# Kernel tuning notes

Measured on AMD Instinct MI355X. Metric: run time of the kernel, lower is better.

The kernel has to match this reference:

```python
import math
import jax, jax.numpy as jnp
import numpy as np

N, B, C, H, K = 1024, 8, 512, 8, 5  # seq len, batch, d_model, heads, near_kth
NEG = -1.0e9


def setup_inputs() -> dict:
    key = jax.random.key(0)
    ks = jax.random.split(key, 10)
    s = 0.02
    return {
        "query": jax.random.normal(ks[0], (N, B, C), jnp.float32),
        "key_t": jax.random.normal(ks[1], (N, B, C), jnp.float32),
        "value": jax.random.normal(ks[2], (N, B, C), jnp.float32),
        "src_position": jax.random.normal(ks[3], (N, B, 3), jnp.float32),
        "tgt_position": jax.random.normal(ks[4], (N, B, 3), jnp.float32),
        # nn.MultiheadAttention params (in_proj split into q/k/v, plus out_proj)
        "Wq": jax.random.normal(ks[5], (C, C), jnp.float32) * s,
        "Wk": jax.random.normal(ks[6], (C, C), jnp.float32) * s,
        "Wv": jax.random.normal(ks[7], (C, C), jnp.float32) * s,
        "bq": jnp.zeros((C,), jnp.float32),
        "bk": jnp.zeros((C,), jnp.float32),
        "bv": jnp.zeros((C,), jnp.float32),
        "Wo": jax.random.normal(ks[8], (C, C), jnp.float32) * s,
        "bo": jnp.zeros((C,), jnp.float32),
    }


def reference(query, key_t, value, src_position, tgt_position,
              Wq, Wk, Wv, bq, bk, bv, Wo, bo):
    # --- 'nearby' positional mask ---------------------------------------
    # dist[b, tgt, src] = ||src_position[src,b] - tgt_position[tgt,b]||^2
    diff = src_position[None, :, :, :] - tgt_position[:, None, :, :]  # (Nt,Ns,B,3)
    dist = jnp.sum(diff * diff, axis=-1).transpose(2, 0, 1)           # (B,Nt,Ns)
    # torch: topk(dist, k=5, dim=1, largest=False) -> 5 nearest TARGETS per source
    _, idx = jax.lax.top_k(-dist.transpose(0, 2, 1), K)               # (B,Ns,K) tgt idx
    mask = jnp.full((B, N, N), NEG, jnp.float32)
    b_i = jnp.arange(B)[:, None, None]
    s_i = jnp.arange(N)[None, :, None]
    mask = mask.at[b_i, idx, s_i].set(0.0)                            # (B,Nt,Ns)

    # --- multihead attention (eval mode, dropout=0) ----------------------
    hd = C // H
    scale = 1.0 / math.sqrt(hd)
    q = ((query @ Wq.T + bq) * scale).reshape(N, B, H, hd)
    k = (key_t @ Wk.T + bk).reshape(N, B, H, hd)
    v = (value @ Wv.T + bv).reshape(N, B, H, hd)
    scores = jnp.einsum('tbhd,sbhd->bhts', q, k) + mask[:, None]      # (B,H,Nt,Ns)
    attn = jax.nn.softmax(scores, axis=-1)
    ctx = jnp.einsum('bhts,sbhd->tbhd', attn, v).reshape(N, B, C)
    out = ctx @ Wo.T + bo                                             # (N,B,C)
    attn_avg = attn.mean(axis=1)                                      # (B,Nt,Ns)
    return out, attn_avg
```

## Files before the change

kernel.cpp:

```cpp
#include <hip/hip_runtime.h>
#include <cstdint>
#include <cstddef>

#define NSEQ 1024
#define BATCH 8
#define CMODEL 512
#define NHEAD 8
#define HDIM 64
#define CAP 64
#define FLTMAX 3.402823466e+38f

typedef short bf16x8 __attribute__((ext_vector_type(8)));
typedef float f32x4 __attribute__((ext_vector_type(4)));
typedef unsigned short ushort8v __attribute__((ext_vector_type(8)));
typedef unsigned short ushort2v __attribute__((ext_vector_type(2)));

__device__ inline unsigned short f2bf(float f) {
    unsigned int u = __builtin_bit_cast(unsigned int, f);
    u += 0x7fffu + ((u >> 16) & 1u);
    return (unsigned short)(u >> 16);
}
__device__ inline float bf2f(unsigned short u) {
    return __builtin_bit_cast(float, (unsigned int)u << 16);
}

#define GLDS16(gsrc, ldst) \
    __builtin_amdgcn_global_load_lds((const __attribute__((address_space(1))) void*)(gsrc), \
                                     (__attribute__((address_space(3))) void*)(ldst), 16, 0, 0)

__global__ __launch_bounds__(256) void convert_all(
        const float* __restrict__ a0, const float* __restrict__ a1,
        const float* __restrict__ a2,
        const float* __restrict__ w0, const float* __restrict__ w1,
        const float* __restrict__ w2, const float* __restrict__ w3,
        unsigned short* __restrict__ oa0, unsigned short* __restrict__ oa1,
        unsigned short* __restrict__ oa2,
        unsigned short* __restrict__ ow0, unsigned short* __restrict__ ow1,
        unsigned short* __restrict__ ow2, unsigned short* __restrict__ ow3,
        unsigned int* __restrict__ zp) {
    const unsigned int idx = blockIdx.x * 256 + threadIdx.x;
    if (idx >= 1703936u) { zp[idx - 1703936u] = 0u; return; }
    const float* src; unsigned short* dst; unsigned int c;
    if (idx < 1572864u) {
        const unsigned int seg = idx >> 19; c = idx & 524287u;
        src = seg == 0 ? a0 : seg == 1 ? a1 : a2;
        dst = seg == 0 ? oa0 : seg == 1 ? oa1 : oa2;
    } else {
        const unsigned int rel = idx - 1572864u, seg = rel >> 15; c = rel & 32767u;
        src = seg == 0 ? w0 : seg == 1 ? w1 : seg == 2 ? w2 : w3;
        dst = seg == 0 ? ow0 : seg == 1 ? ow1 : seg == 2 ? ow2 : ow3;
    }
    const float4 v0 = *(const float4*)(src + (size_t)c * 8);
    const float4 v1 = *(const float4*)(src + (size_t)c * 8 + 4);
    ushort8v u;
    u[0] = f2bf(v0.x); u[1] = f2bf(v0.y); u[2] = f2bf(v0.z); u[3] = f2bf(v0.w);
    u[4] = f2bf(v1.x); u[5] = f2bf(v1.y); u[6] = f2bf(v1.z); u[7] = f2bf(v1.w);
    *(ushort8v*)(dst + (size_t)c * 8) = u;
}

__global__ __launch_bounds__(256) void topk_scatter(const float* __restrict__ srcp,
                                                    const float* __restrict__ tgtp,
                                                    int* __restrict__ row_cnt,
                                                    int* __restrict__ row_list) {
    const int w = threadIdx.x >> 6, lane = threadIdx.x & 63;
    const int wg = blockIdx.x * 4 + w;
    const int s = wg & 1023, b = wg >> 10;

    const float sx = srcp[((size_t)s * BATCH + b) * 3 + 0];
    const float sy = srcp[((size_t)s * BATCH + b) * 3 + 1];
    const float sz = srcp[((size_t)s * BATCH + b) * 3 + 2];

    float dv[16];
    #pragma unroll
    for (int i = 0; i < 16; ++i) {
        const int t = i * 64 + lane;
        const float dx = tgtp[((size_t)t * BATCH + b) * 3 + 0] - sx;
        const float dy = tgtp[((size_t)t * BATCH + b) * 3 + 1] - sy;
        const float dz = tgtp[((size_t)t * BATCH + b) * 3 + 2] - sz;
        dv[i] = dx * dx + dy * dy + dz * dz;
    }

    #pragma unroll
    for (int k = 0; k < 5; ++k) {
        float bvv = FLTMAX;
        int   bii = 0x7fffffff;
        #pragma unroll
        for (int i = 0; i < 16; ++i) {
            if (dv[i] < bvv) { bvv = dv[i]; bii = i * 64 + lane; }
        }
        #pragma unroll
        for (int off = 1; off < 64; off <<= 1) {
            const float ov = __shfl_xor(bvv, off);
            const int   oi = __shfl_xor(bii, off);
            if (ov < bvv || (ov == bvv && oi < bii)) { bvv = ov; bii = oi; }
        }
        if (lane == (bii & 63)) {
            #pragma unroll
            for (int i = 0; i < 16; ++i)
                if (bii == i * 64 + lane) dv[i] = FLTMAX;
        }
        if (lane == 0) {
            const int pos = atomicAdd(&row_cnt[b * NSEQ + bii], 1);
            if (pos < CAP) row_list[((size_t)b * NSEQ + bii) * CAP + pos] = s;
        }
    }
}

template<int OMODE>
__device__ inline void gemm_body(const unsigned short* __restrict__ Abf,
                                 const unsigned short* __restrict__ Wbf,
                                 const float* __restrict__ bias,
                                 void* __restrict__ outp, float scale) {
    __shared__ __align__(16) unsigned short smem[3 * 8192];
    const int tid = threadIdx.x;
    const int l = tid & 63, w = tid >> 6;
    const int m0 = blockIdx.x * 128, n0 = blockIdx.y * 128;
    const int wr = (w >> 1) * 64, wc = (w & 1) * 64;
    const int lr = l & 15, g = l >> 4;

    f32x4 acc[4][4] = {};

    const int rowX = tid >> 2;
    const int kg0  = (tid & 3) ^ ((rowX >> 1) & 3);
    const unsigned short* aS0 = Abf + (size_t)(m0 + rowX) * CMODEL + kg0 * 8;
    const unsigned short* aS1 = aS0 + (size_t)64 * CMODEL;
    const unsigned short* bS0 = Wbf + (size_t)(n0 + rowX) * CMODEL + kg0 * 8;
    const unsigned short* bS1 = bS0 + (size_t)64 * CMODEL;
    const int wb = w * 512;

    auto STAGE = [&](int k0, int buf) {
        unsigned short* bb = smem + buf * 8192;
        GLDS16(aS0 + k0, bb + wb);
        GLDS16(aS1 + k0, bb + 2048 + wb);
        GLDS16(bS0 + k0, bb + 4096 + wb);
        GLDS16(bS1 + k0, bb + 6144 + wb);
    };
    auto COMPUTE = [&](const unsigned short* base) {
        bf16x8 af[4], bg[4];
        #pragma unroll
        for (int i = 0; i < 4; ++i) {
            const int ra = wr + i * 16 + lr;
            af[i] = *(const bf16x8*)(base + ra * 32 + ((g ^ ((ra >> 1) & 3)) << 3));
        }
        #pragma unroll
        for (int j = 0; j < 4; ++j) {
            const int rb = wc + j * 16 + lr;
            bg[j] = *(const bf16x8*)(base + 4096 + rb * 32 + ((g ^ ((rb >> 1) & 3)) << 3));
        }
        __builtin_amdgcn_s_setprio(1);
        #pragma unroll
        for (int i = 0; i < 4; ++i)
            #pragma unroll
            for (int j = 0; j < 4; ++j)
                acc[i][j] = __builtin_amdgcn_mfma_f32_16x16x32_bf16(af[i], bg[j], acc[i][j], 0, 0, 0);
        __builtin_amdgcn_s_setprio(0);
    };

    STAGE(0, 0);
    STAGE(32, 1);

    int cur = 0;
    for (int t = 0; t < 15; ++t) {
        asm volatile("s_waitcnt vmcnt(4)" ::: "memory");
        __builtin_amdgcn_s_barrier();
        if (t < 14) {
            int nb = cur + 2; if (nb >= 3) nb -= 3;
            STAGE((t + 2) * 32, nb);
        }
        COMPUTE(smem + cur * 8192);
        ++cur; if (cur == 3) cur = 0;
    }
    asm volatile("s_waitcnt vmcnt(0)" ::: "memory");
    __builtin_amdgcn_s_barrier();
    COMPUTE(smem + cur * 8192);

    #pragma unroll
    for (int i = 0; i < 4; ++i) {
        #pragma unroll
        for (int j = 0; j < 4; ++j) {
            const int col = n0 + wc + j * 16 + lr;
            const float bcol = bias[col];
            #pragma unroll
            for (int r = 0; r < 4; ++r) {
                const int row = m0 + wr + i * 16 + g * 4 + r;
                const float val = (acc[i][j][r] + bcol) * scale;
                if constexpr (OMODE == 0) {
                    const int t = row >> 3, bb = row & 7;
                    ((unsigned short*)outp)[((size_t)(bb * NSEQ + t)) * CMODEL + col] = f2bf(val);
                } else {
                    ((float*)outp)[(size_t)row * CMODEL + col] = val;
                }
            }
        }
    }
}

__global__ __launch_bounds__(256, 3) void gemm_proj(const unsigned short* __restrict__ Aq,
                                                    const unsigned short* __restrict__ Ak,
                                                    const unsigned short* __restrict__ Av,
                                                    const unsigned short* __restrict__ Wq,
                                                    const unsigned short* __restrict__ Wk,
                                                    const unsigned short* __restrict__ Wv,
                                                    const float* __restrict__ bq,
                                                    const float* __restrict__ bk,
                                                    const float* __restrict__ bv,
                                                    unsigned short* __restrict__ oq,
                                                    unsigned short* __restrict__ ok,
                                                    unsigned short* __restrict__ ov) {
    const int z = blockIdx.z;
    const unsigned short* A = z == 0 ? Aq : z == 1 ? Ak : Av;
    const unsigned short* W = z == 0 ? Wq : z == 1 ? Wk : Wv;
    const float* bi = z == 0 ? bq : z == 1 ? bk : bv;
    unsigned short* o = z == 0 ? oq : z == 1 ? ok : ov;
    const float sc = z == 0 ? 0.125f : 1.0f;
    gemm_body<0>(A, W, bi, o, sc);
}

__global__ __launch_bounds__(256, 3) void gemm_out(const unsigned short* __restrict__ Abf,
                                                   const unsigned short* __restrict__ Wbf,
                                                   const float* __restrict__ bias,
                                                   float* __restrict__ out) {
    gemm_body<1>(Abf, Wbf, bias, out, 1.0f);
}

__global__ __launch_bounds__(512) void v_mean_k(const unsigned short* __restrict__ v,
                                                float* __restrict__ vm) {
    const int b = blockIdx.x;
    const int chunk = blockIdx.y;
    const int c = threadIdx.x;
    float s = 0.f;
    const int t0 = chunk * 64;
    for (int t = 0; t < 64; ++t)
        s += bf2f(v[((size_t)b * NSEQ + t0 + t) * CMODEL + c]);
    atomicAdd(&vm[b * CMODEL + c], s * (1.f / (float)NSEQ));
}

__global__ __launch_bounds__(256) void sparse_attn(const unsigned short* __restrict__ q_ws,
                                                   const unsigned short* __restrict__ k_ws,
                                                   const unsigned short* __restrict__ v_ws,
                                                   const int* __restrict__ row_cnt,
                                                   const int* __restrict__ row_list,
                                                   const float* __restrict__ vm,
                                                   unsigned short* __restrict__ ctx,
                                                   float* __restrict__ attn_out) {
    const int t = blockIdx.x;
    const int b = blockIdx.y;
    const int tid = threadIdx.x;

    int cnt = row_cnt[b * NSEQ + t];
    if (cnt > CAP) cnt = CAP;

    float* arow = attn_out + ((size_t)b * NSEQ + t) * NSEQ;

    if (cnt == 0) {
        const float u = 1.f / (float)NSEQ;
        const float4 uv = {u, u, u, u};
        ((float4*)arow)[tid] = uv;
        for (int c = tid; c < CMODEL; c += 256)
            ctx[((size_t)t * BATCH + b) * CMODEL + c] = f2bf(vm[b * CMODEL + c]);
        return;
    }

    {
        const float4 zv = {0.f, 0.f, 0.f, 0.f};
        ((float4*)arow)[tid] = zv;
    }

    __shared__ float qs[CMODEL];
    __shared__ float esc[CAP][8];
    __shared__ float denom[8];
    __shared__ int   slist[CAP];

    if (tid < 8) denom[tid] = 0.f;
    if (tid < cnt) slist[tid] = row_list[((size_t)b * NSEQ + t) * CAP + tid];
    {
        const ushort2v qv = *(const ushort2v*)(q_ws + ((size_t)b * NSEQ + t) * CMODEL + tid * 2);
        qs[tid * 2] = bf2f(qv[0]); qs[tid * 2 + 1] = bf2f(qv[1]);
    }
    __syncthreads();

    const int wid = tid >> 6, lane = tid & 63;
    for (int i = wid; i < cnt; i += 4) {
        const int s = slist[i];
        const ushort8v kv = *(const ushort8v*)(k_ws + ((size_t)b * NSEQ + s) * CMODEL + lane * 8);
        const float* qrow = qs + lane * 8;
        float part = 0.f;
        #pragma unroll
        for (int j = 0; j < 8; ++j) part += qrow[j] * bf2f(kv[j]);
        part += __shfl_xor(part, 1);
        part += __shfl_xor(part, 2);
        part += __shfl_xor(part, 4);
        if ((lane & 7) == 0) {
            const int h = lane >> 3;
            const float e = __expf(part);
            esc[i][h] = e;
            atomicAdd(&denom[h], e);
        }
    }
    __syncthreads();

    for (int x = tid; x < cnt * 8; x += 256)
        esc[x >> 3][x & 7] /= denom[x & 7];
    __syncthreads();

    for (int i = tid; i < cnt; i += 256) {
        float pm = 0.f;
        #pragma unroll
        for (int h = 0; h < 8; ++h) pm += esc[i][h];
        arow[slist[i]] = pm * 0.125f;
    }

    const int c0 = tid * 2;
    const int h0 = c0 >> 6;
    float acc0 = 0.f, acc1 = 0.f;
    for (int i = 0; i < cnt; ++i) {
        const int s = slist[i];
        const float p = esc[i][h0];
        const ushort2v vv = *(const ushort2v*)(v_ws + ((size_t)b * NSEQ + s) * CMODEL + c0);
        acc0 += p * bf2f(vv[0]); acc1 += p * bf2f(vv[1]);
    }
    unsigned short* crow = ctx + ((size_t)t * BATCH + b) * CMODEL;
    ushort2v cv; cv[0] = f2bf(acc0); cv[1] = f2bf(acc1);
    *(ushort2v*)(crow + c0) = cv;
}

extern "C" void kernel_launch(void* const* d_in, const int* in_sizes, int n_in,
                              void* d_out, int out_size, void* d_ws, size_t ws_size,
                              hipStream_t stream) {
    (void)in_sizes; (void)n_in; (void)out_size; (void)ws_size;

    const float* query = (const float*)d_in[0];
    const float* key_t = (const float*)d_in[1];
    const float* value = (const float*)d_in[2];
    const float* srcp  = (const float*)d_in[3];
    const float* tgtp  = (const float*)d_in[4];
    const float* Wq    = (const float*)d_in[5];
    const float* Wk    = (const float*)d_in[6];
    const float* Wv    = (const float*)d_in[7];
    const float* bq    = (const float*)d_in[8];
    const float* bk    = (const float*)d_in[9];
    const float* bv    = (const float*)d_in[10];
    const float* Wo    = (const float*)d_in[11];
    const float* bo    = (const float*)d_in[12];

    float* out      = (float*)d_out;
    float* attn_out = out + (size_t)NSEQ * BATCH * CMODEL;

    const size_t NBC = (size_t)BATCH * NSEQ * CMODEL;
    const size_t WSZ = (size_t)CMODEL * CMODEL;
    unsigned short* q_ws  = (unsigned short*)d_ws;
    unsigned short* k_ws  = q_ws + NBC;
    unsigned short* v_ws  = k_ws + NBC;
    unsigned short* ctxbf = v_ws + NBC;
    unsigned short* qbf   = ctxbf + NBC;
    unsigned short* kbf   = qbf + NBC;
    unsigned short* vbf   = kbf + NBC;
    unsigned short* wqbf  = vbf + NBC;
    unsigned short* wkbf  = wqbf + WSZ;
    unsigned short* wvbf  = wkbf + WSZ;
    unsigned short* wobf  = wvbf + WSZ;
    int*   row_cnt  = (int*)(wobf + WSZ);
    float* vm       = (float*)(row_cnt + BATCH * NSEQ);
    int*   row_list = (int*)(vm + BATCH * CMODEL);

    convert_all<<<6704, 256, 0, stream>>>(query, key_t, value, Wq, Wk, Wv, Wo,
                                          qbf, kbf, vbf, wqbf, wkbf, wvbf, wobf,
                                          (unsigned int*)row_cnt);

    topk_scatter<<<2048, 256, 0, stream>>>(srcp, tgtp, row_cnt, row_list);

    gemm_proj<<<dim3(64, 4, 3), 256, 0, stream>>>(qbf, kbf, vbf,
                                                  wqbf, wkbf, wvbf,
                                                  bq, bk, bv,
                                                  q_ws, k_ws, v_ws);

    v_mean_k<<<dim3(BATCH, 16), 512, 0, stream>>>(v_ws, vm);

    sparse_attn<<<dim3(NSEQ, BATCH), 256, 0, stream>>>(q_ws, k_ws, v_ws, row_cnt,
                                                       row_list, vm, ctxbf, attn_out);

    gemm_out<<<dim3(64, 4), 256, 0, stream>>>(ctxbf, wobf, bo, out);
}
```

Before: 90.86 us.

## Fuse fp32-to-bf16 activation conversion into projection GEMM and fold V-mean

Drops the separate conversion pass over query/key/value activations. The projection GEMM now loads fp32 A tiles into registers, converts them to bf16 and writes them to LDS, while the weights are still staged through async global-to-LDS loads. The mean of V is no longer read back from the projected output. Instead the prep kernel reduces the raw fp32 value over the sequence, and an extra column of GEMM blocks multiplies that mean by Wv. This removes one full-tensor write and read plus a kernel launch, at the cost of register-path A loads, an lgkmcnt wait before every barrier, and a changed rounding of the V mean.

```diff
diff --git a/kernel.cpp b/kernel.cpp
--- a/kernel.cpp
+++ b/kernel.cpp
@@ -28,34 +28,51 @@
     __builtin_amdgcn_global_load_lds((const __attribute__((address_space(1))) void*)(gsrc), \
                                      (__attribute__((address_space(3))) void*)(ldst), 16, 0, 0)
 
-__global__ __launch_bounds__(256) void convert_all(
-        const float* __restrict__ a0, const float* __restrict__ a1,
-        const float* __restrict__ a2,
-        const float* __restrict__ w0, const float* __restrict__ w1,
-        const float* __restrict__ w2, const float* __restrict__ w3,
-        unsigned short* __restrict__ oa0, unsigned short* __restrict__ oa1,
-        unsigned short* __restrict__ oa2,
-        unsigned short* __restrict__ ow0, unsigned short* __restrict__ ow1,
-        unsigned short* __restrict__ ow2, unsigned short* __restrict__ ow3,
-        unsigned int* __restrict__ zp) {
-    const unsigned int idx = blockIdx.x * 256 + threadIdx.x;
-    if (idx >= 1703936u) { zp[idx - 1703936u] = 0u; return; }
-    const float* src; unsigned short* dst; unsigned int c;
-    if (idx < 1572864u) {
-        const unsigned int seg = idx >> 19; c = idx & 524287u;
-        src = seg == 0 ? a0 : seg == 1 ? a1 : a2;
-        dst = seg == 0 ? oa0 : seg == 1 ? oa1 : oa2;
-    } else {
-        const unsigned int rel = idx - 1572864u, seg = rel >> 15; c = rel & 32767u;
-        src = seg == 0 ? w0 : seg == 1 ? w1 : seg == 2 ? w2 : w3;
-        dst = seg == 0 ? ow0 : seg == 1 ? ow1 : seg == 2 ? ow2 : ow3;
-    }
-    const float4 v0 = *(const float4*)(src + (size_t)c * 8);
-    const float4 v1 = *(const float4*)(src + (size_t)c * 8 + 4);
-    ushort8v u;
-    u[0] = f2bf(v0.x); u[1] = f2bf(v0.y); u[2] = f2bf(v0.z); u[3] = f2bf(v0.w);
-    u[4] = f2bf(v1.x); u[5] = f2bf(v1.y); u[6] = f2bf(v1.z); u[7] = f2bf(v1.w);
-    *(ushort8v*)(dst + (size_t)c * 8) = u;
+__global__ __launch_bounds__(256) void prep(const float* __restrict__ w0,
+                                            const float* __restrict__ w1,
+                                            const float* __restrict__ w2,
+                                            const float* __restrict__ w3,
+                                            const float* __restrict__ value,
+                                            unsigned short* __restrict__ o0,
+                                            unsigned short* __restrict__ o1,
+                                            unsigned short* __restrict__ o2,
+                                            unsigned short* __restrict__ o3,
+                                            unsigned int* __restrict__ zp,
+                                            float* __restrict__ vm_raw) {
+    const int bid = blockIdx.x;
+    const int tid = threadIdx.x;
+    if (bid < 512) {
+        const int idx = bid * 256 + tid;
+        const int seg = idx >> 15;
+        const int c   = idx & 32767;
+        const float* src = seg == 0 ? w0 : seg == 1 ? w1 : seg == 2 ? w2 : w3;
+        unsigned short* dst = seg == 0 ? o0 : seg == 1 ? o1 : seg == 2 ? o2 : o3;
+        const float4 v0 = *(const float4*)(src + (size_t)c * 8);
+        const float4 v1 = *(const float4*)(src + (size_t)c * 8 + 4);
+        ushort8v u;
+        u[0] = f2bf(v0.x); u[1] = f2bf(v0.y); u[2] = f2bf(v0.z); u[3] = f2bf(v0.w);
+        u[4] = f2bf(v1.x); u[5] = f2bf(v1.y); u[6] = f2bf(v1.z); u[7] = f2bf(v1.w);
+        *(ushort8v*)(dst + (size_t)c * 8) = u;
+        return;
+    }
+    if (bid < 544) {
+        zp[(bid - 512) * 256 + tid] = 0u;
+        return;
+    }
+    const int cb = bid - 544;
+    const int b = cb >> 3, cg = cb & 7;
+    const int ts = tid >> 6, c = cg * 64 + (tid & 63);
+    float s = 0.f;
+    for (int i = 0; i < 256; ++i) {
+        const int t = ts * 256 + i;
+        s += value[((size_t)t * BATCH + b) * CMODEL + c];
+    }
+    __shared__ float sh[4][64];
+    sh[ts][tid & 63] = s;
+    __syncthreads();
+    if (ts == 0)
+        vm_raw[b * CMODEL + c] = sh[0][tid & 63] + sh[1][tid & 63] +
+                                 sh[2][tid & 63] + sh[3][tid & 63];
 }
 
 __global__ __launch_bounds__(256) void topk_scatter(const float* __restrict__ srcp,
@@ -106,11 +123,11 @@
     }
 }
 
-template<int OMODE>
-__device__ inline void gemm_body(const unsigned short* __restrict__ Abf,
-                                 const unsigned short* __restrict__ Wbf,
-                                 const float* __restrict__ bias,
-                                 void* __restrict__ outp, float scale) {
+__device__ inline void gemm_fp32A_body(const float* __restrict__ A,
+                                       const unsigned short* __restrict__ Wbf,
+                                       const float* __restrict__ bias,
+                                       unsigned short* __restrict__ outp,
+                                       float scale) {
     __shared__ __align__(16) unsigned short smem[3 * 8192];
     const int tid = threadIdx.x;
     const int l = tid & 63, w = tid >> 6;
@@ -120,20 +137,36 @@
 
     f32x4 acc[4][4] = {};
 
-    const int rowX = tid >> 2;
-    const int kg0  = (tid & 3) ^ ((rowX >> 1) & 3);
-    const unsigned short* aS0 = Abf + (size_t)(m0 + rowX) * CMODEL + kg0 * 8;
-    const unsigned short* aS1 = aS0 + (size_t)64 * CMODEL;
-    const unsigned short* bS0 = Wbf + (size_t)(n0 + rowX) * CMODEL + kg0 * 8;
+    const int rowA = tid >> 2;
+    const int slA  = tid & 3;
+    const int sw   = (rowA >> 1) & 3;
+    const float* aS0 = A + (size_t)(m0 + rowA) * CMODEL + slA * 8;
+    const float* aS1 = aS0 + (size_t)64 * CMODEL;
+    const int adst0 = rowA * 32 + (slA ^ sw) * 8;
+    const int adst1 = adst0 + 64 * 32;
+    const unsigned short* bS0 = Wbf + (size_t)(n0 + rowA) * CMODEL + (slA ^ sw) * 8;
     const unsigned short* bS1 = bS0 + (size_t)64 * CMODEL;
     const int wb = w * 512;
 
-    auto STAGE = [&](int k0, int buf) {
+    float4 a0, a1, a2, a3;
+    auto LOADA = [&](int k0) {
+        a0 = *(const float4*)(aS0 + k0); a1 = *(const float4*)(aS0 + k0 + 4);
+        a2 = *(const float4*)(aS1 + k0); a3 = *(const float4*)(aS1 + k0 + 4);
+    };
+    auto CVT_WRITE = [&](int buf) {
+        ushort8v u0, u1;
+        u0[0] = f2bf(a0.x); u0[1] = f2bf(a0.y); u0[2] = f2bf(a0.z); u0[3] = f2bf(a0.w);
+        u0[4] = f2bf(a1.x); u0[5] = f2bf(a1.y); u0[6] = f2bf(a1.z); u0[7] = f2bf(a1.w);
+        u1[0] = f2bf(a2.x); u1[1] = f2bf(a2.y); u1[2] = f2bf(a2.z); u1[3] = f2bf(a2.w);
+        u1[4] = f2bf(a3.x); u1[5] = f2bf(a3.y); u1[6] = f2bf(a3.z); u1[7] = f2bf(a3.w);
         unsigned short* bb = smem + buf * 8192;
-        GLDS16(aS0 + k0, bb + wb);
-        GLDS16(aS1 + k0, bb + 2048 + wb);
-        GLDS16(bS0 + k0, bb + 4096 + wb);
-        GLDS16(bS1 + k0, bb + 6144 + wb);
+        *(ushort8v*)(bb + adst0) = u0;
+        *(ushort8v*)(bb + adst1) = u1;
+    };
+    auto STAGE_B = [&](int k0, int buf) {
+        unsigned short* bb = smem + buf * 8192 + 4096;
+        GLDS16(bS0 + k0, bb + wb);
+        GLDS16(bS1 + k0, bb + 2048 + wb);
     };
     auto COMPUTE = [&](const unsigned short* base) {
         bf16x8 af[4], bg[4];
@@ -156,23 +189,28 @@
         __builtin_amdgcn_s_setprio(0);
     };
 
-    STAGE(0, 0);
-    STAGE(32, 1);
-
-    int cur = 0;
-    for (int t = 0; t < 15; ++t) {
-        asm volatile("s_waitcnt vmcnt(4)" ::: "memory");
+    LOADA(0);
+    STAGE_B(0, 0);
+    CVT_WRITE(0);
+    LOADA(32);
+    STAGE_B(32, 1);
+
+    for (int t = 0; t < 16; ++t) {
+        const int cur = t % 3;
+        if (t < 15) {
+            CVT_WRITE((t + 1) % 3);
+        } else {
+            asm volatile("s_waitcnt vmcnt(0)" ::: "memory");
+        }
+        asm volatile("s_waitcnt lgkmcnt(0)" ::: "memory");
+        __builtin_amdgcn_sched_barrier(0);
         __builtin_amdgcn_s_barrier();
         if (t < 14) {
-            int nb = cur + 2; if (nb >= 3) nb -= 3;
-            STAGE((t + 2) * 32, nb);
+            LOADA((t + 2) * 32);
+            STAGE_B((t + 2) * 32, (t + 2) % 3);
         }
         COMPUTE(smem + cur * 8192);
-        ++cur; if (cur == 3) cur = 0;
-    }
-    asm volatile("s_waitcnt vmcnt(0)" ::: "memory");
-    __builtin_amdgcn_s_barrier();
-    COMPUTE(smem + cur * 8192);
+    }
 
     #pragma unroll
     for (int i = 0; i < 4; ++i) {
@@ -184,20 +222,16 @@
             for (int r = 0; r < 4; ++r) {
                 const int row = m0 + wr + i * 16 + g * 4 + r;
                 const float val = (acc[i][j][r] + bcol) * scale;
-                if constexpr (OMODE == 0) {
-                    const int t = row >> 3, bb = row & 7;
-                    ((unsigned short*)outp)[((size_t)(bb * NSEQ + t)) * CMODEL + col] = f2bf(val);
-                } else {
-                    ((float*)outp)[(size_t)row * CMODEL + col] = val;
-                }
+                const int t = row >> 3, bb = row & 7;
+                outp[((size_t)(bb * NSEQ + t)) * CMODEL + col] = f2bf(val);
             }
         }
     }
 }
 
-__global__ __launch_bounds__(256, 3) void gemm_proj(const unsigned short* __restrict__ Aq,
-                                                    const unsigned short* __restrict__ Ak,
-                                                    const unsigned short* __restrict__ Av,
+__global__ __launch_bounds__(256, 3) void gemm_proj(const float* __restrict__ Aq,
+                                                    const float* __restrict__ Ak,
+                                                    const float* __restrict__ Av,
                                                     const unsigned short* __restrict__ Wq,
                                                     const unsigned short* __restrict__ Wk,
                                                     const unsigned short* __restrict__ Wv,
@@ -206,33 +240,115 @@
                                                     const float* __restrict__ bv,
                                                     unsigned short* __restrict__ oq,
                                                     unsigned short* __restrict__ ok,
-                                                    unsigned short* __restrict__ ov) {
+                                                    unsigned short* __restrict__ ov,
+                                                    const float* __restrict__ vm_raw,
+                                                    float* __restrict__ vm) {
+    if (blockIdx.x == 64) {
+        const int bsel = blockIdx.z * 4 + blockIdx.y;
+        if (bsel >= BATCH) return;
+        const int c0 = threadIdx.x * 2;
+        float s0 = 0.f, s1 = 0.f;
+        const unsigned short* w0r = Wv + (size_t)c0 * CMODEL;
+        const unsigned short* w1r = w0r + CMODEL;
+        const float* vr = vm_raw + bsel * CMODEL;
+        for (int k = 0; k < CMODEL; ++k) {
+            const float v = vr[k];
+            s0 += v * bf2f(w0r[k]);
+            s1 += v * bf2f(w1r[k]);
+        }
+        vm[bsel * CMODEL + c0]     = s0 * (1.f / (float)NSEQ) + bv[c0];
+        vm[bsel * CMODEL + c0 + 1] = s1 * (1.f / (float)NSEQ) + bv[c0 + 1];
+        return;
+    }
     const int z = blockIdx.z;
-    const unsigned short* A = z == 0 ? Aq : z == 1 ? Ak : Av;
+    const float* A = z == 0 ? Aq : z == 1 ? Ak : Av;
     const unsigned short* W = z == 0 ? Wq : z == 1 ? Wk : Wv;
     const float* bi = z == 0 ? bq : z == 1 ? bk : bv;
     unsigned short* o = z == 0 ? oq : z == 1 ? ok : ov;
     const float sc = z == 0 ? 0.125f : 1.0f;
-    gemm_body<0>(A, W, bi, o, sc);
+    gemm_fp32A_body(A, W, bi, o, sc);
 }
 
 __global__ __launch_bounds__(256, 3) void gemm_out(const unsigned short* __restrict__ Abf,
                                                    const unsigned short* __restrict__ Wbf,
                                                    const float* __restrict__ bias,
                                                    float* __restrict__ out) {
-    gemm_body<1>(Abf, Wbf, bias, out, 1.0f);
-}
-
-__global__ __launch_bounds__(512) void v_mean_k(const unsigned short* __restrict__ v,
-                                                float* __restrict__ vm) {
-    const int b = blockIdx.x;
-    const int chunk = blockIdx.y;
-    const int c = threadIdx.x;
-    float s = 0.f;
-    const int t0 = chunk * 64;
-    for (int t = 0; t < 64; ++t)
-        s += bf2f(v[((size_t)b * NSEQ + t0 + t) * CMODEL + c]);
-    atomicAdd(&vm[b * CMODEL + c], s * (1.f / (float)NSEQ));
+    __shared__ __align__(16) unsigned short smem[3 * 8192];
+    const int tid = threadIdx.x;
+    const int l = tid & 63, w = tid >> 6;
+    const int m0 = blockIdx.x * 128, n0 = blockIdx.y * 128;
+    const int wr = (w >> 1) * 64, wc = (w & 1) * 64;
+    const int lr = l & 15, g = l >> 4;
+
+    f32x4 acc[4][4] = {};
+
+    const int rowX = tid >> 2;
+    const int kg0  = (tid & 3) ^ ((rowX >> 1) & 3);
+    const unsigned short* aS0 = Abf + (size_t)(m0 + rowX) * CMODEL + kg0 * 8;
+    const unsigned short* aS1 = aS0 + (size_t)64 * CMODEL;
+    const unsigned short* bS0 = Wbf + (size_t)(n0 + rowX) * CMODEL + kg0 * 8;
+    const unsigned short* bS1 = bS0 + (size_t)64 * CMODEL;
+    const int wb = w * 512;
+
+    auto STAGE = [&](int k0, int buf) {
+        unsigned short* bb = smem + buf * 8192;
+        GLDS16(aS0 + k0, bb + wb);
+        GLDS16(aS1 + k0, bb + 2048 + wb);
+        GLDS16(bS0 + k0, bb + 4096 + wb);
+        GLDS16(bS1 + k0, bb + 6144 + wb);
+    };
+    auto COMPUTE = [&](const unsigned short* base) {
+        bf16x8 af[4], bg[4];
+        #pragma unroll
+        for (int i = 0; i < 4; ++i) {
+            const int ra = wr + i * 16 + lr;
+            af[i] = *(const bf16x8*)(base + ra * 32 + ((g ^ ((ra >> 1) & 3)) << 3));
+        }
+        #pragma unroll
+        for (int j = 0; j < 4; ++j) {
+            const int rb = wc + j * 16 + lr;
+            bg[j] = *(const bf16x8*)(base + 4096 + rb * 32 + ((g ^ ((rb >> 1) & 3)) << 3));
+        }
+        __builtin_amdgcn_s_setprio(1);
+        #pragma unroll
+        for (int i = 0; i < 4; ++i)
+            #pragma unroll
+            for (int j = 0; j < 4; ++j)
+                acc[i][j] = __builtin_amdgcn_mfma_f32_16x16x32_bf16(af[i], bg[j], acc[i][j], 0, 0, 0);
+        __builtin_amdgcn_s_setprio(0);
+    };
+
+    STAGE(0, 0);
+    STAGE(32, 1);
+
+    int cur = 0;
+    for (int t = 0; t < 15; ++t) {
+        asm volatile("s_waitcnt vmcnt(4)" ::: "memory");
+        __builtin_amdgcn_s_barrier();
+        if (t < 14) {
+            int nb = cur + 2; if (nb >= 3) nb -= 3;
+            STAGE((t + 2) * 32, nb);
+        }
+        COMPUTE(smem + cur * 8192);
+        ++cur; if (cur == 3) cur = 0;
+    }
+    asm volatile("s_waitcnt vmcnt(0)" ::: "memory");
+    __builtin_amdgcn_s_barrier();
+    COMPUTE(smem + cur * 8192);
+
+    #pragma unroll
+    for (int i = 0; i < 4; ++i) {
+        #pragma unroll
+        for (int j = 0; j < 4; ++j) {
+            const int col = n0 + wc + j * 16 + lr;
+            const float bcol = bias[col];
+            #pragma unroll
+            for (int r = 0; r < 4; ++r) {
+                const int row = m0 + wr + i * 16 + g * 4 + r;
+                out[(size_t)row * CMODEL + col] = acc[i][j][r] + bcol;
+            }
+        }
+    }
 }
 
 __global__ __launch_bounds__(256) void sparse_attn(const unsigned short* __restrict__ q_ws,
@@ -352,29 +468,26 @@
     unsigned short* k_ws  = q_ws + NBC;
     unsigned short* v_ws  = k_ws + NBC;
     unsigned short* ctxbf = v_ws + NBC;
-    unsigned short* qbf   = ctxbf + NBC;
-    unsigned short* kbf   = qbf + NBC;
-    unsigned short* vbf   = kbf + NBC;
-    unsigned short* wqbf  = vbf + NBC;
+    unsigned short* wqbf  = ctxbf + NBC;
     unsigned short* wkbf  = wqbf + WSZ;
     unsigned short* wvbf  = wkbf + WSZ;
     unsigned short* wobf  = wvbf + WSZ;
     int*   row_cnt  = (int*)(wobf + WSZ);
     float* vm       = (float*)(row_cnt + BATCH * NSEQ);
-    int*   row_list = (int*)(vm + BATCH * CMODEL);
-
-    convert_all<<<6704, 256, 0, stream>>>(query, key_t, value, Wq, Wk, Wv, Wo,
-                                          qbf, kbf, vbf, wqbf, wkbf, wvbf, wobf,
-                                          (unsigned int*)row_cnt);
+    float* vm_raw   = vm + BATCH * CMODEL;
+    int*   row_list = (int*)(vm_raw + BATCH * CMODEL);
+
+    prep<<<608, 256, 0, stream>>>(Wq, Wk, Wv, Wo, value,
+                                  wqbf, wkbf, wvbf, wobf,
+                                  (unsigned int*)row_cnt, vm_raw);
 
     topk_scatter<<<2048, 256, 0, stream>>>(srcp, tgtp, row_cnt, row_list);
 
-    gemm_proj<<<dim3(64, 4, 3), 256, 0, stream>>>(qbf, kbf, vbf,
+    gemm_proj<<<dim3(65, 4, 3), 256, 0, stream>>>(query, key_t, value,
                                                   wqbf, wkbf, wvbf,
                                                   bq, bk, bv,
-                                                  q_ws, k_ws, v_ws);
-
-    v_mean_k<<<dim3(BATCH, 16), 512, 0, stream>>>(v_ws, vm);
+                                                  q_ws, k_ws, v_ws,
+                                                  vm_raw, vm);
 
     sparse_attn<<<dim3(NSEQ, BATCH), 256, 0, stream>>>(q_ws, k_ws, v_ws, row_cnt,
                                                        row_list, vm, ctxbf, attn_out);
```

New measurement: 110.1 us. 1.21x slower.
